# Kernel optimization log

Measured on AMD Instinct MI355X. Metric: run time of the kernel, lower is better.

## Reference

```python
import jax, jax.numpy as jnp
import numpy as np

B, L, H, D, TXT = 128, 512, 336, 256, 768
K, S, EMB = 16, 4, 128
H_SCALE = 0.15
EPS, ITERS = 0.05, 30
ALPHA, BETA = 1.0, 0.5
GW, TAU = 0.5, 0.07
LMB_MSE, LMB_COT, LMB_DELTA, LMB_ENT, LMB_TV = 1.0, 0.1, 0.1, 0.01, 0.01


def setup_inputs() -> dict:
    key = jax.random.key(0)
    ks = jax.random.split(key, 12)
    def xav(k, shape):
        return jax.random.normal(k, shape, jnp.float32) / np.sqrt(shape[0]).astype(np.float32)
    inp = {}
    inp['y_res'] = jax.random.normal(ks[0], (B, H, D), jnp.float32)
    inp['text_emb'] = jax.random.normal(ks[1], (B, TXT), jnp.float32)
    inp['enc_out'] = jax.random.normal(ks[2], (B, L, D), jnp.float32)
    inp['y_future'] = jax.random.normal(ks[3], (B, H, D), jnp.float32)
    inp['perm'] = jax.random.permutation(ks[4], EMB)
    inp['W_t2k'] = xav(ks[5], (TXT, K * (3 + S))); inp['b_t2k'] = jnp.zeros((K * (3 + S),), jnp.float32)
    inp['W_kemb'] = xav(ks[6], (H, EMB)); inp['b_kemb'] = jnp.zeros((EMB,), jnp.float32)
    inp['W_tir'] = xav(ks[7], (1, D)); inp['b_tir'] = jnp.zeros((D,), jnp.float32)
    inp['var_proj'] = jnp.ones((D,), jnp.float32)
    inp['W_g1'] = xav(ks[8], (2 * D + TXT, 512)); inp['b_g1'] = jnp.zeros((512,), jnp.float32)
    inp['W_g2'] = xav(ks[9], (512, D)); inp['b_g2'] = jnp.zeros((D,), jnp.float32)
    inp['W_fp'] = xav(ks[10], (3 * D, EMB)); inp['b_fp'] = jnp.zeros((EMB,), jnp.float32)
    return inp


def _text2kernels(text_emb, W, b):
    # text -> K temporal kernels: mixture of S shape bases with learned mu/sigma/amp
    raw = (text_emb @ W + b).reshape(-1, K, 3 + S)
    mu = jax.nn.sigmoid(raw[..., 0])                       # [B,K] center in [0,1]
    sig = jax.nn.softplus(raw[..., 1]) * H_SCALE + 1e-3     # [B,K] width
    amp = jax.nn.softplus(raw[..., 2])                      # [B,K]
    shape_w = jax.nn.softmax(raw[..., 3:], axis=-1)         # [B,K,S]
    t = (jnp.arange(H, dtype=text_emb.dtype) + 0.5) / H     # [H]
    z = (t[None, None, :] - mu[..., None]) / sig[..., None]  # [B,K,H]
    az = jnp.abs(z)
    in_supp = (az <= 1.0).astype(z.dtype)
    basis = jnp.stack([
        jnp.exp(-0.5 * z * z),
        jnp.exp(-az),
        jnp.maximum(1.0 - az, 0.0),
        0.5 * (1.0 + jnp.cos(jnp.pi * jnp.clip(z, -1.0, 1.0))) * in_supp,
    ], axis=-1)                                             # [B,K,H,S]
    kappa = amp[..., None] * jnp.einsum('bkhs,bks->bkh', basis, shape_w)
    return kappa, mu, shape_w


def _future_proj(y, W, b):
    # concat(y, first diff, second diff) -> linear, in_dim = 3*D
    d1 = jnp.diff(y, axis=1, prepend=y[:, :1])
    d2 = jnp.diff(d1, axis=1, prepend=d1[:, :1])
    return jnp.concatenate([y, d1, d2], axis=-1) @ W + b    # [B,H,EMB]


def _l2n(x):
    return x / (jnp.linalg.norm(x, axis=-1, keepdims=True) + 1e-8)


def _causal_cost(k_emb, f_pos, mu):
    cossim = jnp.einsum('bkd,bhd->bkh', _l2n(k_emb), _l2n(f_pos))
    t = (jnp.arange(H, dtype=k_emb.dtype) + 0.5) / H
    causal = jnp.maximum(mu[:, :, None] - t[None, None, :], 0.0)  # effect-before-cause penalty
    return ALPHA * (1.0 - cossim) + BETA * causal            # [B,K,H]


def _sinkhorn(C, r, c):
    Kmat = jnp.exp(-C / EPS)
    def body(i, uv):
        u, v = uv
        u = r / (jnp.einsum('bkh,bh->bk', Kmat, v) + 1e-9)
        v = c / (jnp.einsum('bkh,bk->bh', Kmat, u) + 1e-9)
        return (u, v)
    u, v = jax.lax.fori_loop(0, ITERS, body, (jnp.ones_like(r), jnp.ones_like(c)))
    return u[:, :, None] * Kmat * v[:, None, :]              # [B,K,H]


def _delta_contrastive(k_emb, f_pos, Pi, negatives):
    w = Pi / (jnp.sum(Pi, axis=-1, keepdims=True) + 1e-9)    # transport-weighted aggregation
    kn = _l2n(k_emb)
    def sim(f):
        return jnp.einsum('bkd,bkd->bk', kn, _l2n(jnp.einsum('bkh,bhd->bkd', w, f)))
    logits = jnp.stack([sim(f_pos)] + [sim(f) for f in negatives], axis=-1) / TAU  # [B,K,1+neg]
    return -jnp.mean(jax.nn.log_softmax(logits, axis=-1)[..., 0])


def reference(y_res, text_emb, enc_out, y_future, perm, W_t2k, b_t2k, W_kemb, b_kemb,
              W_tir, b_tir, var_proj, W_g1, b_g1, W_g2, b_g2, W_fp, b_fp):
    # --- text-induced response ---
    kappa, mu, shape_w = _text2kernels(text_emb, W_t2k, b_t2k)   # [B,K,H]
    y_tir_scalar = kappa.sum(axis=1)                             # [B,H]
    # --- gated fusion ---
    y_tir = (y_tir_scalar[..., None] @ W_tir + b_tir) * var_proj[None, None, :]  # [B,H,D]
    ts_global = enc_out.mean(axis=1)                             # [B,D]
    gate_in = jnp.concatenate([ts_global, text_emb, jnp.broadcast_to(var_proj[None, :], (y_res.shape[0], D))], axis=-1)
    gate = jax.nn.sigmoid(jax.nn.relu(gate_in @ W_g1 + b_g1) @ W_g2 + b_g2)[:, None, :]  # [B,1,D]
    y_hat = y_res + GW * gate * (y_tir - y_res)
    # --- aux losses ---
    k_emb = kappa @ W_kemb + b_kemb                              # [B,K,EMB]
    f_pos = _future_proj(y_future, W_fp, b_fp)                   # [B,H,EMB]
    C = _causal_cost(k_emb, f_pos, mu)
    r = jax.lax.stop_gradient(kappa.sum(-1) + 1e-6)
    r = r / r.sum(axis=-1, keepdims=True)
    c = jnp.full((C.shape[0], C.shape[2]), 1.0 / C.shape[2], C.dtype)
    Pi = _sinkhorn(C, r, c)
    shift = max(1, H // 6)
    f_neg1 = jnp.roll(f_pos, shift, axis=1)
    f_neg2 = f_pos[..., perm]
    loss_delta = _delta_contrastive(k_emb, f_pos, Pi, [f_neg1, f_neg2])
    loss_cot = jnp.mean(jnp.sum(C * Pi, axis=(1, 2)))
    sw = jnp.maximum(shape_w, 1e-8)
    loss_ent = -jnp.mean(jnp.sum(sw * jnp.log(sw), axis=-1))
    loss_tv = jnp.mean(jnp.abs(mu[:, 1:] - mu[:, :-1]))
    loss_mse = jnp.mean((y_hat - y_future) ** 2)
    return (LMB_MSE * loss_mse + LMB_COT * loss_cot + LMB_DELTA * loss_delta
            + LMB_ENT * loss_ent + LMB_TV * loss_tv)
```

## Files before the change

kernel.cpp:

```cpp
#include <hip/hip_runtime.h>
#include <math.h>

#define Bn   128
#define Ln   512
#define Hn   336
#define Dn   256
#define TXTn 768
#define Kn   16
#define EMBn 128
#define SHIFT 56
#define MSEB 1024
#define FROWS 48
#define FTILES 7
#define ASTRIDE 776

typedef __attribute__((ext_vector_type(8))) short short8;
typedef __attribute__((ext_vector_type(4))) float floatx4;

__device__ __forceinline__ float softplusf(float x){
  return fmaxf(x, 0.f) + log1pf(expf(-fabsf(x)));
}
__device__ __forceinline__ unsigned short f2bf(float x){
  unsigned int u = __float_as_uint(x);
  unsigned int r = (u + 0x7fffu + ((u >> 16) & 1u)) >> 16;
  return (unsigned short)r;
}
__device__ __forceinline__ float rcpf(float x){ return __builtin_amdgcn_rcpf(x); }
__device__ __forceinline__ float wsum(float x){
  x += __shfl_xor(x, 1);  x += __shfl_xor(x, 2);  x += __shfl_xor(x, 4);
  x += __shfl_xor(x, 8);  x += __shfl_xor(x, 16); x += __shfl_xor(x, 32);
  return x;
}

__global__ __launch_bounds__(256) void k_fused1(
    const float* __restrict__ text, const float* __restrict__ W, const float* __restrict__ bb,
    float* __restrict__ mu_o, float* __restrict__ kapT, float* __restrict__ rr_o,
    float* __restrict__ ytirs, float* __restrict__ part_ent, float* __restrict__ part_tv){
  int b = blockIdx.x, t = threadIdx.x;
  __shared__ float kapS[Kn*Hn];
  __shared__ float musL[Kn], sigL[Kn], ampL[Kn], shwL[Kn*4], entS[Kn], rrS[Kn];
  __shared__ float red[256];
  __shared__ float comb[112];
  __shared__ float totS;
  {
    int o = t & 127, half = t >> 7;
    if (o < 112){
      const float* tb = text + (size_t)b*TXTn + half*384;
      const float* Wb = W + (size_t)half*384*112 + o;
      float a0=0.f, a1=0.f, a2=0.f, a3=0.f;
      for (int i = 0; i < 384; i += 4){
        float4 x = *(const float4*)(tb + i);
        a0 += x.x*Wb[(i+0)*112]; a1 += x.y*Wb[(i+1)*112];
        a2 += x.z*Wb[(i+2)*112]; a3 += x.w*Wb[(i+3)*112];
      }
      red[half*112 + o] = (a0 + a1) + (a2 + a3);
    }
  }
  __syncthreads();
  if (t < 112) comb[t] = red[t] + red[112 + t] + bb[t];
  __syncthreads();
  if (t < Kn){
    float r0 = comb[t*7+0], r1 = comb[t*7+1], r2 = comb[t*7+2];
    float mu  = 1.f/(1.f+expf(-r0));
    float sig = softplusf(r1)*0.15f + 1e-3f;
    float amp = softplusf(r2);
    float s0 = comb[t*7+3], s1 = comb[t*7+4], s2 = comb[t*7+5], s3 = comb[t*7+6];
    float m = fmaxf(fmaxf(s0,s1), fmaxf(s2,s3));
    float e0 = expf(s0-m), e1 = expf(s1-m), e2 = expf(s2-m), e3 = expf(s3-m);
    float inv = 1.f/(e0+e1+e2+e3);
    float w0 = e0*inv, w1 = e1*inv, w2 = e2*inv, w3 = e3*inv;
    musL[t] = mu; sigL[t] = sig; ampL[t] = amp;
    shwL[t*4+0] = w0; shwL[t*4+1] = w1; shwL[t*4+2] = w2; shwL[t*4+3] = w3;
    mu_o[b*Kn + t] = mu;
    float ent = 0.f, sw;
    sw = fmaxf(w0,1e-8f); ent += sw*logf(sw);
    sw = fmaxf(w1,1e-8f); ent += sw*logf(sw);
    sw = fmaxf(w2,1e-8f); ent += sw*logf(sw);
    sw = fmaxf(w3,1e-8f); ent += sw*logf(sw);
    entS[t] = ent;
  }
  __syncthreads();
  for (int p = t; p < Kn*Hn; p += 256){
    int k = p/Hn, h = p - k*Hn;
    float mu = musL[k], sig = sigL[k], amp = ampL[k];
    float w0 = shwL[k*4+0], w1 = shwL[k*4+1], w2 = shwL[k*4+2], w3 = shwL[k*4+3];
    float tt = (h + 0.5f)/(float)Hn;
    float z  = (tt - mu)/sig;
    float az = fabsf(z);
    float b0 = expf(-0.5f*z*z);
    float b1 = expf(-az);
    float b2 = fmaxf(1.f-az, 0.f);
    float zc = fminf(fmaxf(z,-1.f),1.f);
    float b3 = (az <= 1.f) ? 0.5f*(1.f+cosf(3.14159265358979f*zc)) : 0.f;
    kapS[p] = amp*(w0*b0 + w1*b1 + w2*b2 + w3*b3);
  }
  __syncthreads();
  for (int q = t; q < Kn*Hn; q += 256){
    int h = q >> 4, k = q & 15;
    kapT[((size_t)b*Hn + h)*Kn + k] = kapS[k*Hn + h];
  }
  {
    int k = t >> 4, j16 = t & 15;
    float s = 0.f;
    for (int h = j16; h < Hn; h += 16) s += kapS[k*Hn + h];
    red[t] = s;
  }
  __syncthreads();
  if (t < Kn){
    float s = 0.f;
    for (int j = 0; j < 16; ++j) s += red[t*16 + j];
    rrS[t] = s + 1e-6f;
  }
  __syncthreads();
  if (t == 0){
    float tot = 0.f, tv = 0.f, es = 0.f;
    for (int k = 0; k < Kn; ++k) tot += rrS[k];
    for (int k = 1; k < Kn; ++k) tv += fabsf(musL[k]-musL[k-1]);
    for (int k = 0; k < Kn; ++k) es += entS[k];
    totS = tot; part_tv[b] = tv; part_ent[b] = es;
  }
  __syncthreads();
  if (t < Kn) rr_o[b*Kn + t] = rrS[t]/totS;
  for (int h = t; h < Hn; h += 256){
    float s = 0.f;
    #pragma unroll
    for (int k = 0; k < Kn; ++k) s += kapS[k*Hn + h];
    ytirs[b*Hn + h] = s;
  }
}

__global__ __launch_bounds__(128) void k_kemb1(const float* __restrict__ kapT,
    const float* __restrict__ W, float* __restrict__ kp){
  int blk = blockIdx.x;
  int b = blk >> 3, oc = blk & 7;
  int e = threadIdx.x;
  float acc[Kn];
  #pragma unroll
  for (int k = 0; k < Kn; ++k) acc[k] = 0.f;
  const float* kb = kapT + (size_t)b*Hn*Kn;
  int h0 = oc*42, h1 = h0 + 42;
  for (int h = h0; h < h1; ++h){
    float wv = W[h*EMBn + e];
    const float4* kr = (const float4*)(kb + h*Kn);
    float4 c0 = kr[0], c1 = kr[1], c2 = kr[2], c3 = kr[3];
    acc[0]  += c0.x*wv; acc[1]  += c0.y*wv; acc[2]  += c0.z*wv; acc[3]  += c0.w*wv;
    acc[4]  += c1.x*wv; acc[5]  += c1.y*wv; acc[6]  += c1.z*wv; acc[7]  += c1.w*wv;
    acc[8]  += c2.x*wv; acc[9]  += c2.y*wv; acc[10] += c2.z*wv; acc[11] += c2.w*wv;
    acc[12] += c3.x*wv; acc[13] += c3.y*wv; acc[14] += c3.z*wv; acc[15] += c3.w*wv;
  }
  float* kpb = kp + ((size_t)blk*Kn)*EMBn + e;
  #pragma unroll
  for (int k = 0; k < Kn; ++k) kpb[(size_t)k*EMBn] = acc[k];
}

__global__ __launch_bounds__(256) void k_kemb2(const float* __restrict__ kp,
    const float* __restrict__ bb, float* __restrict__ kn_o){
  int b = blockIdx.x, t = threadIdx.x;
  __shared__ float kS[Kn*EMBn];
  __shared__ float r2[256];
  __shared__ float invS[Kn];
  for (int j = t; j < Kn*EMBn; j += 256){
    int e = j & 127;
    float s = bb[e];
    const float* p = kp + (size_t)b*8*Kn*EMBn + j;
    #pragma unroll
    for (int oc = 0; oc < 8; ++oc) s += p[(size_t)oc*Kn*EMBn];
    kS[j] = s;
  }
  __syncthreads();
  {
    int k = t & 15, g = t >> 4;
    float s = 0.f;
    for (int e = g; e < EMBn; e += 16){ float v = kS[k*EMBn + e]; s += v*v; }
    r2[g*Kn + k] = s;
  }
  __syncthreads();
  if (t < Kn){
    float s = 0.f;
    for (int g = 0; g < 16; ++g) s += r2[g*Kn + t];
    invS[t] = 1.f/(sqrtf(s) + 1e-8f);
  }
  __syncthreads();
  for (int j = t; j < Kn*EMBn; j += 256)
    kn_o[(size_t)b*Kn*EMBn + j] = kS[j]*invS[j >> 7];
}

__global__ void k_wprep(const float* __restrict__ W, unsigned short* __restrict__ Bsw){
  int tid = blockIdx.x*256 + threadIdx.x;
  int k = tid >> 7, n = tid & 127;
  int kt = k >> 5, kr = k & 31, quad = kr >> 3, j = kr & 7;
  int c = n >> 4, ln = n & 15;
  int lane = quad*16 + ln;
  int dst = ((kt*8 + c)*64 + lane)*8 + j;
  Bsw[dst] = f2bf(W[k*128 + n]);
}

__global__ __launch_bounds__(256) void k_encmean(const float* __restrict__ enc,
                                                 float* __restrict__ psum){
  int blk = blockIdx.x;
  int b = blk >> 3, p = blk & 7;
  int t = threadIdx.x;
  int d4 = t & 63, rg = t >> 6;
  const float4* e4 = (const float4*)(enc + (size_t)b*Ln*Dn);
  float4 s = make_float4(0.f,0.f,0.f,0.f);
  for (int l = p + 8*rg; l < Ln; l += 32){
    float4 v = e4[(size_t)l*64 + d4];
    s.x += v.x; s.y += v.y; s.z += v.z; s.w += v.w;
  }
  __shared__ float4 red[256];
  red[t] = s;
  __syncthreads();
  if (rg == 0){
    float4 o = red[d4];
    #pragma unroll
    for (int r = 1; r < 4; ++r){
      float4 v = red[r*64 + d4];
      o.x += v.x; o.y += v.y; o.z += v.z; o.w += v.w;
    }
    ((float4*)(psum + ((size_t)b*8 + p)*Dn))[d4] = o;
  }
}

__global__ __launch_bounds__(256) void k_gmlp1(const float* __restrict__ psum,
    const float* __restrict__ text, const float* __restrict__ vp,
    const float* __restrict__ W1, float* __restrict__ hidp){
  int bt = blockIdx.x >> 5, hc = (blockIdx.x >> 2) & 7, ks = blockIdx.x & 3;
  int t = threadIdx.x;
  __shared__ float inS[4][320];
  for (int j = t; j < 4*320; j += 256){
    int bi = j / 320, jj = j - bi*320;
    int gi = ks*320 + jj;
    int b = bt*4 + bi;
    float vsl;
    if (gi < Dn){
      float s = 0.f;
      for (int p = 0; p < 8; ++p) s += psum[((size_t)b*8 + p)*Dn + gi];
      vsl = s * (1.f/(float)Ln);
    } else if (gi < Dn + TXTn){
      vsl = text[(size_t)b*TXTn + (gi - Dn)];
    } else {
      vsl = vp[gi - Dn - TXTn];
    }
    inS[bi][jj] = vsl;
  }
  __syncthreads();
  int h = t & 63, bi = t >> 6;
  int hidx = hc*64 + h;
  const float* Wb = W1 + (size_t)(ks*320)*512 + hidx;
  float a0 = 0.f, a1 = 0.f, a2 = 0.f, a3 = 0.f;
  const float4* in4 = (const float4*)inS[bi];
  for (int i = 0; i < 320; i += 4){
    float4 x = in4[i >> 2];
    a0 += x.x*Wb[(size_t)(i+0)*512]; a1 += x.y*Wb[(size_t)(i+1)*512];
    a2 += x.z*Wb[(size_t)(i+2)*512]; a3 += x.w*Wb[(size_t)(i+3)*512];
  }
  hidp[((size_t)ks*Bn + bt*4 + bi)*512 + hidx] = (a0 + a1) + (a2 + a3);
}

__global__ __launch_bounds__(256) void k_gmlp2(const float* __restrict__ hidp,
    const float* __restrict__ b1, const float* __restrict__ W2,
    const float* __restrict__ b2, float* __restrict__ gate_o){
  int bt = blockIdx.x >> 3, dc = blockIdx.x & 7;
  int t = threadIdx.x;
  __shared__ float hS[4][512];
  __shared__ float pS[8][4][32];
  for (int j = t; j < 4*512; j += 256){
    int bi = j >> 9, i = j & 511;
    size_t bidx = (size_t)(bt*4 + bi)*512 + i;
    float s = hidp[bidx] + hidp[(size_t)Bn*512 + bidx]
            + hidp[(size_t)2*Bn*512 + bidx] + hidp[(size_t)3*Bn*512 + bidx];
    hS[bi][i] = fmaxf(s + b1[i], 0.f);
  }
  __syncthreads();
  {
    int dl = t & 31, ig = t >> 5;
    int d  = dc*32 + dl;
    float a0=0.f, a1=0.f, a2=0.f, a3=0.f;
    int i0 = ig*64;
    for (int i = i0; i < i0 + 64; ++i){
      float wv = W2[(size_t)i*Dn + d];
      a0 += hS[0][i]*wv; a1 += hS[1][i]*wv;
      a2 += hS[2][i]*wv; a3 += hS[3][i]*wv;
    }
    pS[ig][0][dl] = a0; pS[ig][1][dl] = a1;
    pS[ig][2][dl] = a2; pS[ig][3][dl] = a3;
  }
  __syncthreads();
  if (t < 128){
    int bi = t >> 5, dl = t & 31;
    float s = 0.f;
    #pragma unroll
    for (int g = 0; g < 8; ++g) s += pS[g][bi][dl];
    s += b2[dc*32 + dl];
    gate_o[(size_t)(bt*4 + bi)*Dn + dc*32 + dl] = 1.f/(1.f + expf(-s));
  }
}

__global__ __launch_bounds__(256) void k_fposm(const float* __restrict__ yf,
    const unsigned short* __restrict__ Bsw, const float* __restrict__ bb,
    float* __restrict__ fpos, float* __restrict__ finv){
  int b = blockIdx.x / FTILES, tile = blockIdx.x % FTILES;
  int t = threadIdx.x;
  int h0 = tile*FROWS;
  __shared__ unsigned short yS[FROWS*ASTRIDE];
  __shared__ float rsq[4][FROWS];
  const float* yb = yf + (size_t)b*Hn*Dn;

  #pragma unroll
  for (int u = 0; u < 12; ++u){
    int unit = t + 256*u;
    int r = unit >> 6, d4 = unit & 63;
    int h = h0 + r;
    int hm1 = h-1 < 0 ? 0 : h-1;
    int hm2 = h-2 < 0 ? 0 : h-2;
    float4 y   = *(const float4*)(yb + (size_t)h  *Dn + d4*4);
    float4 ym1 = *(const float4*)(yb + (size_t)hm1*Dn + d4*4);
    float4 ym2 = *(const float4*)(yb + (size_t)hm2*Dn + d4*4);
    float4 d1 = make_float4(y.x-ym1.x, y.y-ym1.y, y.z-ym1.z, y.w-ym1.w);
    float4 d2 = make_float4(y.x-2.f*ym1.x+ym2.x, y.y-2.f*ym1.y+ym2.y,
                            y.z-2.f*ym1.z+ym2.z, y.w-2.f*ym1.w+ym2.w);
    union { unsigned short u16[4]; uint2 v; } p;
    unsigned short* base = &yS[r*ASTRIDE + d4*4];
    p.u16[0]=f2bf(y.x);  p.u16[1]=f2bf(y.y);  p.u16[2]=f2bf(y.z);  p.u16[3]=f2bf(y.w);
    *(uint2*)(base)        = p.v;
    p.u16[0]=f2bf(d1.x); p.u16[1]=f2bf(d1.y); p.u16[2]=f2bf(d1.z); p.u16[3]=f2bf(d1.w);
    *(uint2*)(base + 256)  = p.v;
    p.u16[0]=f2bf(d2.x); p.u16[1]=f2bf(d2.y); p.u16[2]=f2bf(d2.z); p.u16[3]=f2bf(d2.w);
    *(uint2*)(base + 512)  = p.v;
  }
  __syncthreads();

  int wv   = __builtin_amdgcn_readfirstlane(t >> 6);
  int lane = t & 63, quad = lane >> 4, ln = lane & 15;
  int c0 = wv*2;
  floatx4 acc[3][2];
  #pragma unroll
  for (int i = 0; i < 3; ++i){
    acc[i][0] = (floatx4){0.f,0.f,0.f,0.f};
    acc[i][1] = (floatx4){0.f,0.f,0.f,0.f};
  }
  #pragma unroll
  for (int kt = 0; kt < 24; ++kt){
    int aoff = kt*32 + quad*8;
    short8 a0 = *(const short8*)&yS[( 0 + ln)*ASTRIDE + aoff];
    short8 a1 = *(const short8*)&yS[(16 + ln)*ASTRIDE + aoff];
    short8 a2 = *(const short8*)&yS[(32 + ln)*ASTRIDE + aoff];
    short8 b0 = *(const short8*)&Bsw[((kt*8 + c0  )*64 + lane)*8];
    short8 b1 = *(const short8*)&Bsw[((kt*8 + c0+1)*64 + lane)*8];
    acc[0][0] = __builtin_amdgcn_mfma_f32_16x16x32_bf16(a0, b0, acc[0][0], 0, 0, 0);
    acc[0][1] = __builtin_amdgcn_mfma_f32_16x16x32_bf16(a0, b1, acc[0][1], 0, 0, 0);
    acc[1][0] = __builtin_amdgcn_mfma_f32_16x16x32_bf16(a1, b0, acc[1][0], 0, 0, 0);
    acc[1][1] = __builtin_amdgcn_mfma_f32_16x16x32_bf16(a1, b1, acc[1][1], 0, 0, 0);
    acc[2][0] = __builtin_amdgcn_mfma_f32_16x16x32_bf16(a2, b0, acc[2][0], 0, 0, 0);
    acc[2][1] = __builtin_amdgcn_mfma_f32_16x16x32_bf16(a2, b1, acc[2][1], 0, 0, 0);
  }

  float bias0 = bb[c0*16 + ln], bias1 = bb[(c0+1)*16 + ln];
  #pragma unroll
  for (int rt = 0; rt < 3; ++rt){
    #pragma unroll
    for (int reg = 0; reg < 4; ++reg){
      int lrow = rt*16 + quad*4 + reg;
      size_t row = (size_t)b*Hn + h0 + lrow;
      float v0 = acc[rt][0][reg] + bias0;
      float v1 = acc[rt][1][reg] + bias1;
      fpos[row*EMBn + c0*16 + ln]     = v0;
      fpos[row*EMBn + (c0+1)*16 + ln] = v1;
      float sq = v0*v0 + v1*v1;
      sq += __shfl_xor(sq, 1); sq += __shfl_xor(sq, 2);
      sq += __shfl_xor(sq, 4); sq += __shfl_xor(sq, 8);
      if (ln == 0) rsq[wv][lrow] = sq;
    }
  }
  __syncthreads();
  if (t < FROWS){
    float s = rsq[0][t] + rsq[1][t] + rsq[2][t] + rsq[3][t];
    finv[(size_t)b*Hn + h0 + t] = 1.f/(sqrtf(s) + 1e-8f);
  }
}

__global__ void k_mse(const float* __restrict__ yres, const float* __restrict__ yfut,
                      const float* __restrict__ gate, const float* __restrict__ ytirs,
                      const float* __restrict__ Wt, const float* __restrict__ bt,
                      const float* __restrict__ vp, float* __restrict__ part_mse){
  const long long total = (long long)Bn*Hn*Dn;
  long long tid = blockIdx.x*(long long)blockDim.x + threadIdx.x;
  long long nth = gridDim.x*(long long)blockDim.x;
  float part = 0.f;
  for (long long i4 = tid; i4*4 < total; i4 += nth){
    long long base = i4*4;
    int b = (int)(base/((long long)Hn*Dn));
    int rem = (int)(base - (long long)b*Hn*Dn);
    int h = rem/Dn, d = rem - h*Dn;
    float4 yr = *(const float4*)(yres + base);
    float4 yv = *(const float4*)(yfut + base);
    float4 g  = *(const float4*)(gate + (size_t)b*Dn + d);
    float4 wt = *(const float4*)(Wt + d);
    float4 bv = *(const float4*)(bt + d);
    float4 vv = *(const float4*)(vp + d);
    float ys = ytirs[b*Hn + h];
    float yt, yh, e;
    yt = (ys*wt.x + bv.x)*vv.x; yh = yr.x + 0.5f*g.x*(yt-yr.x); e = yh-yv.x; part += e*e;
    yt = (ys*wt.y + bv.y)*vv.y; yh = yr.y + 0.5f*g.y*(yt-yr.y); e = yh-yv.y; part += e*e;
    yt = (ys*wt.z + bv.z)*vv.z; yh = yr.z + 0.5f*g.z*(yt-yr.z); e = yh-yv.z; part += e*e;
    yt = (ys*wt.w + bv.w)*vv.w; yh = yr.w + 0.5f*g.w*(yt-yr.w); e = yh-yv.w; part += e*e;
  }
  __shared__ float red[256];
  red[threadIdx.x] = part; __syncthreads();
  for (int s = 128; s > 0; s >>= 1){
    if (threadIdx.x < s) red[threadIdx.x] += red[threadIdx.x + s];
    __syncthreads();
  }
  if (threadIdx.x == 0) part_mse[blockIdx.x] = red[0];
}

__global__ __launch_bounds__(256) void k_cost(const float* __restrict__ kn,
    const float* __restrict__ fpos, const float* __restrict__ finv,
    const float* __restrict__ mu_i, float* __restrict__ Km_g){
  int b = blockIdx.x >> 2, q = blockIdx.x & 3;
  int t = threadIdx.x;
  __shared__ float knS[Kn*132];
  __shared__ float musS[Kn];
  for (int j = t; j < Kn*EMBn; j += 256){
    int k = j >> 7, e = j & 127;
    knS[k*132 + e] = kn[(size_t)b*Kn*EMBn + j];
  }
  if (t < Kn) musS[t] = mu_i[b*Kn + t];
  __syncthreads();
  const int H0 = q*84;
  for (int p = t; p < Kn*84; p += 256){
    int k = p & 15, h = H0 + (p >> 4);
    const float4* f4 = (const float4*)(fpos + ((size_t)b*Hn + h)*EMBn);
    const float4* k4 = (const float4*)(knS + k*132);
    float s = 0.f;
    #pragma unroll 8
    for (int i = 0; i < EMBn/4; ++i){
      float4 a = k4[i], f = f4[i];
      s += a.x*f.x + a.y*f.y + a.z*f.z + a.w*f.w;
    }
    float cs = s*finv[b*Hn + h];
    float th = (h + 0.5f)/(float)Hn;
    float c  = (1.f - cs) + 0.5f*fmaxf(musS[k] - th, 0.f);
    Km_g[(size_t)b*Kn*Hn + k*Hn + h] = expf(-20.f*c);
  }
}

__global__ __launch_bounds__(128) void k_sink1w(const float* __restrict__ rr,
    float* KmwT, float* __restrict__ part_cot){
  int b = blockIdx.x, t = threadIdx.x;
  int l = t & 63;
  float* Kb = KmwT + (size_t)b*Kn*Hn;
  int ks = ((l&1)<<3) | ((l&2)<<1) | ((l&4)>>1) | ((l&8)>>3);
  __shared__ float ws[128];
  float km[16][3];
  #pragma unroll
  for (int m = 0; m < 16; ++m){
    const float* rowp = Kb + (size_t)(ks ^ m)*Hn;
    #pragma unroll
    for (int c = 0; c < 3; ++c){
      int h = 128*c + t;
      km[m][c] = (h < Hn) ? rowp[h] : 0.f;
    }
  }
  float rrl = rr[b*Kn + ks];
  float v[3];
  v[0] = 1.f; v[1] = 1.f; v[2] = 1.f;
  float w[16];
  for (int it = 0; it < 30; ++it){
    float p[16];
    #pragma unroll
    for (int m = 0; m < 16; ++m)
      p[m] = km[m][0]*v[0] + km[m][1]*v[1] + km[m][2]*v[2];
    #pragma unroll
    for (int m = 0; m < 8; ++m) p[m] += __shfl_xor(p[m+8], 1);
    #pragma unroll
    for (int m = 0; m < 4; ++m) p[m] += __shfl_xor(p[m+4], 2);
    #pragma unroll
    for (int m = 0; m < 2; ++m) p[m] += __shfl_xor(p[m+2], 4);
    p[0] += __shfl_xor(p[1], 8);
    p[0] += __shfl_xor(p[0], 16);
    p[0] += __shfl_xor(p[0], 32);
    ws[t] = p[0];
    __syncthreads();
    float ptot = ws[l] + ws[64 + l];
    __syncthreads();
    float ul = rrl * rcpf(ptot + 1e-9f);
    w[0] = ul;
    w[1] = __shfl_xor(w[0], 8);
    w[2] = __shfl_xor(w[0], 4); w[3] = __shfl_xor(w[1], 4);
    #pragma unroll
    for (int j = 0; j < 4; ++j) w[4+j] = __shfl_xor(w[j], 2);
    #pragma unroll
    for (int j = 0; j < 8; ++j) w[8+j] = __shfl_xor(w[j], 1);
    #pragma unroll
    for (int c = 0; c < 3; ++c){
      float s0 = 0.f, s1 = 0.f;
      #pragma unroll
      for (int m = 0; m < 8; ++m){ s0 += km[m][c]*w[m]; s1 += km[m+8][c]*w[m+8]; }
      v[c] = (1.f/(float)Hn) * rcpf(s0 + s1 + 1e-9f);
    }
  }
  float q[16];
  #pragma unroll
  for (int m = 0; m < 16; ++m)
    q[m] = km[m][0]*v[0] + km[m][1]*v[1] + km[m][2]*v[2];
  #pragma unroll
  for (int m = 0; m < 8; ++m) q[m] += __shfl_xor(q[m+8], 1);
  #pragma unroll
  for (int m = 0; m < 4; ++m) q[m] += __shfl_xor(q[m+4], 2);
  #pragma unroll
  for (int m = 0; m < 2; ++m) q[m] += __shfl_xor(q[m+2], 4);
  q[0] += __shfl_xor(q[1], 8);
  q[0] += __shfl_xor(q[0], 16);
  q[0] += __shfl_xor(q[0], 32);
  ws[t] = q[0];
  __syncthreads();
  float qtot = ws[l] + ws[64 + l];
  __syncthreads();
  float tt[16];
  tt[0] = qtot;
  tt[1] = __shfl_xor(tt[0], 8);
  tt[2] = __shfl_xor(tt[0], 4); tt[3] = __shfl_xor(tt[1], 4);
  #pragma unroll
  for (int j = 0; j < 4; ++j) tt[4+j] = __shfl_xor(tt[j], 2);
  #pragma unroll
  for (int j = 0; j < 8; ++j) tt[8+j] = __shfl_xor(tt[j], 1);
  float cot = 0.f;
  #pragma unroll
  for (int m = 0; m < 16; ++m){
    float rsinv = rcpf(w[m]*tt[m] + 1e-9f);
    float* rowp = Kb + (size_t)(ks ^ m)*Hn;
    #pragma unroll
    for (int c = 0; c < 3; ++c){
      int h = 128*c + t;
      if (h < Hn){
        float Pi = w[m]*km[m][c]*v[c];
        cot += (-0.05f)*logf(km[m][c])*Pi;
        rowp[h] = Pi*rsinv;
      }
    }
  }
  cot = wsum(cot);
  ws[t] = cot;
  __syncthreads();
  if (t == 0) part_cot[b] = ws[0] + ws[64];
}

__global__ __launch_bounds__(256) void k_agg(const float* __restrict__ kn,
    const float* __restrict__ fpos, const float* __restrict__ wT,
    const int* __restrict__ perm, float* __restrict__ part_del4){
  int b = blockIdx.x >> 2, kg = blockIdx.x & 3;
  int t = threadIdx.x;
  __shared__ float wTl[Hn*4];
  __shared__ float apH[2][4*EMBn];
  __shared__ float a1H[2][4*EMBn];
  __shared__ int permS[EMBn];
  __shared__ float redW[4];
  if (t < EMBn) permS[t] = perm[t];
  for (int j = t; j < 4*Hn; j += 256){
    int k = j & 3, h = j >> 2;
    wTl[h*4 + k] = wT[(size_t)b*Kn*Hn + (size_t)(kg*4 + k)*Hn + h];
  }
  __syncthreads();

  {
    int e = t & 127, jh = t >> 7;
    float ap[4], a1[4];
    #pragma unroll
    for (int j = 0; j < 4; ++j){ ap[j] = 0.f; a1[j] = 0.f; }
    const float* fb = fpos + (size_t)b*Hn*EMBn + e;
    int hh0 = jh*168, hh1 = hh0 + 168;
    for (int h = hh0; h < hh1; ++h){
      float fv = fb[(size_t)h*EMBn];
      int h1 = h + SHIFT; if (h1 >= Hn) h1 -= Hn;
      float4 wA = *(const float4*)&wTl[h *4];
      float4 wB = *(const float4*)&wTl[h1*4];
      ap[0] += wA.x*fv; ap[1] += wA.y*fv; ap[2] += wA.z*fv; ap[3] += wA.w*fv;
      a1[0] += wB.x*fv; a1[1] += wB.y*fv; a1[2] += wB.z*fv; a1[3] += wB.w*fv;
    }
    #pragma unroll
    for (int j = 0; j < 4; ++j){
      apH[jh][j*EMBn + e] = ap[j];
      a1H[jh][j*EMBn + e] = a1[j];
    }
  }
  __syncthreads();
  for (int j = t; j < 4*EMBn; j += 256){
    apH[0][j] += apH[1][j];
    a1H[0][j] += a1H[1][j];
  }
  __syncthreads();

  int wave = t >> 6, lane = t & 63;
  {
    int kl = wave;
    int k  = kg*4 + kl;
    float sp = 0.f, s1 = 0.f, s2 = 0.f, np = 0.f, n1 = 0.f;
    for (int e = lane; e < EMBn; e += 64){
      float kne = kn[((size_t)b*Kn + k)*EMBn + e];
      float a  = apH[0][kl*EMBn + e];
      float c1 = a1H[0][kl*EMBn + e];
      sp += kne*a; s1 += kne*c1;
      s2 += kne*apH[0][kl*EMBn + permS[e]];
      np += a*a; n1 += c1*c1;
    }
    for (int o = 32; o; o >>= 1){
      sp += __shfl_down(sp, o); s1 += __shfl_down(s1, o); s2 += __shfl_down(s2, o);
      np += __shfl_down(np, o); n1 += __shfl_down(n1, o);
    }
    if (lane == 0){
      float ip  = 1.f/(sqrtf(np) + 1e-8f);
      float i1v = 1.f/(sqrtf(n1) + 1e-8f);
      const float ti = 1.f/0.07f;
      float l0 = sp*ip*ti, l1 = s1*i1v*ti, l2 = s2*ip*ti;
      float m = fmaxf(l0, fmaxf(l1, l2));
      float lse = m + logf(expf(l0-m) + expf(l1-m) + expf(l2-m));
      redW[wave] = lse - l0;
    }
  }
  __syncthreads();
  if (t == 0) part_del4[(size_t)b*4 + kg] = redW[0] + redW[1] + redW[2] + redW[3];
}

__global__ void k_final(const float* __restrict__ part_mse, const float* __restrict__ part_cot,
                        const float* __restrict__ part_del4, const float* __restrict__ part_ent,
                        const float* __restrict__ part_tv, float* __restrict__ out){
  int t = threadIdx.x;
  __shared__ double sred[256];
  double m = 0.0;
  for (int i = t; i < MSEB; i += 256) m += (double)part_mse[i];
  double o4 = 0.0;
  if (t < Bn){
    double del = (double)part_del4[4*t] + (double)part_del4[4*t + 1]
               + (double)part_del4[4*t + 2] + (double)part_del4[4*t + 3];
    o4 = 0.1*(double)part_cot[t] + (0.1/(double)Kn)*del
       - (0.01/(double)Kn)*(double)part_ent[t] + (0.01/(double)(Kn-1))*(double)part_tv[t];
  }
  sred[t] = m/((double)Bn*Hn*Dn) + o4/(double)Bn;
  __syncthreads();
  for (int s = 128; s > 0; s >>= 1){ if (t < s) sred[t] += sred[t+s]; __syncthreads(); }
  if (t == 0) out[0] = (float)sred[0];
}

extern "C" void kernel_launch(void* const* d_in, const int* in_sizes, int n_in,
                              void* d_out, int out_size, void* d_ws, size_t ws_size,
                              hipStream_t stream) {
  const float* y_res  = (const float*)d_in[0];
  const float* text   = (const float*)d_in[1];
  const float* enc    = (const float*)d_in[2];
  const float* yfut   = (const float*)d_in[3];
  const int*   perm   = (const int*)  d_in[4];
  const float* W_t2k  = (const float*)d_in[5];
  const float* b_t2k  = (const float*)d_in[6];
  const float* W_kemb = (const float*)d_in[7];
  const float* b_kemb = (const float*)d_in[8];
  const float* W_tir  = (const float*)d_in[9];
  const float* b_tir  = (const float*)d_in[10];
  const float* vproj  = (const float*)d_in[11];
  const float* W_g1   = (const float*)d_in[12];
  const float* b_g1   = (const float*)d_in[13];
  const float* W_g2   = (const float*)d_in[14];
  const float* b_g2   = (const float*)d_in[15];
  const float* W_fp   = (const float*)d_in[16];
  const float* b_fp   = (const float*)d_in[17];

  float* F = (float*)d_ws;
  float* mu_w   = F;
  float* rr_w   = F + 2048;
  float* ytr_w  = F + 4096;
  float* kapT_w = F + 47104;
  float* kn_w   = F + 735232;
  float* gate_w = F + 997376;
  float* fp_w   = F + 1030144;
  float* fi_w   = F + 6535168;
  float* pmse_w = F + 6578176;
  float* pcot_w = F + 6579200;
  float* pent_w = F + 6579456;
  float* ptv_w  = F + 6579584;
  unsigned short* Bsw_w = (unsigned short*)kapT_w;
  float* KmwT_w = kapT_w;
  float* kp_w   = fp_w;
  float* psum_w = fp_w;
  float* hidp_w = fp_w + 262144;
  float* pdel4_w = gate_w;

  k_fused1 <<<Bn, 256, 0, stream>>>(text, W_t2k, b_t2k, mu_w, kapT_w, rr_w, ytr_w, pent_w, ptv_w);
  k_kemb1  <<<Bn*8, 128, 0, stream>>>(kapT_w, W_kemb, kp_w);
  k_kemb2  <<<Bn, 256, 0, stream>>>(kp_w, b_kemb, kn_w);
  k_wprep  <<<384, 256, 0, stream>>>(W_fp, Bsw_w);
  k_encmean<<<Bn*8, 256, 0, stream>>>(enc, psum_w);
  k_gmlp1  <<<1024, 256, 0, stream>>>(psum_w, text, vproj, W_g1, hidp_w);
  k_gmlp2  <<<256, 256, 0, stream>>>(hidp_w, b_g1, W_g2, b_g2, gate_w);
  k_fposm  <<<Bn*FTILES, 256, 0, stream>>>(yfut, Bsw_w, b_fp, fp_w, fi_w);
  k_mse    <<<MSEB, 256, 0, stream>>>(y_res, yfut, gate_w, ytr_w, W_tir, b_tir, vproj, pmse_w);
  k_cost   <<<Bn*4, 256, 0, stream>>>(kn_w, fp_w, fi_w, mu_w, KmwT_w);
  k_sink1w <<<Bn, 128, 0, stream>>>(rr_w, KmwT_w, pcot_w);
  k_agg    <<<Bn*4, 256, 0, stream>>>(kn_w, fp_w, KmwT_w, perm, pdel4_w);
  k_final  <<<1, 256, 0, stream>>>(pmse_w, pcot_w, pdel4_w, pent_w, ptv_w, (float*)d_out);
}
```

Before: 346.0 us.

## Merge independent kernels into multi-role launches to cut launch count

Independent kernels are grouped into combined launches that branch on block index: kemb normalization, weight swizzle and encoder mean share one launch; gate MLP layer 1 and the future projection MFMA share another; gate layer 2 and the cost computation share a third; MSE and the contrastive aggregation share a fourth. This cuts the launch count from 13 to 8 and lets unrelated work overlap on the GPU. Scratch buffers for psum, hidp and pdel4 move to dedicated workspace regions so the merged stages no longer alias each other. The merged launches size shared memory for the largest role, which may lower occupancy for the smaller roles.

```diff
diff --git a/kernel.cpp b/kernel.cpp
--- a/kernel.cpp
+++ b/kernel.cpp
@@ -153,295 +153,260 @@
   for (int k = 0; k < Kn; ++k) kpb[(size_t)k*EMBn] = acc[k];
 }
 
-__global__ __launch_bounds__(256) void k_kemb2(const float* __restrict__ kp,
-    const float* __restrict__ bb, float* __restrict__ kn_o){
-  int b = blockIdx.x, t = threadIdx.x;
+__global__ __launch_bounds__(256) void k_p3(const float* __restrict__ kp,
+    const float* __restrict__ bkemb, float* __restrict__ kn_o,
+    const float* __restrict__ Wfp, unsigned short* __restrict__ Bsw,
+    const float* __restrict__ enc, float* __restrict__ psum){
+  int blk = blockIdx.x, t = threadIdx.x;
   __shared__ float kS[Kn*EMBn];
   __shared__ float r2[256];
   __shared__ float invS[Kn];
-  for (int j = t; j < Kn*EMBn; j += 256){
-    int e = j & 127;
-    float s = bb[e];
-    const float* p = kp + (size_t)b*8*Kn*EMBn + j;
-    #pragma unroll
-    for (int oc = 0; oc < 8; ++oc) s += p[(size_t)oc*Kn*EMBn];
-    kS[j] = s;
-  }
-  __syncthreads();
-  {
-    int k = t & 15, g = t >> 4;
-    float s = 0.f;
-    for (int e = g; e < EMBn; e += 16){ float v = kS[k*EMBn + e]; s += v*v; }
-    r2[g*Kn + k] = s;
-  }
-  __syncthreads();
-  if (t < Kn){
-    float s = 0.f;
-    for (int g = 0; g < 16; ++g) s += r2[g*Kn + t];
-    invS[t] = 1.f/(sqrtf(s) + 1e-8f);
-  }
-  __syncthreads();
-  for (int j = t; j < Kn*EMBn; j += 256)
-    kn_o[(size_t)b*Kn*EMBn + j] = kS[j]*invS[j >> 7];
-}
-
-__global__ void k_wprep(const float* __restrict__ W, unsigned short* __restrict__ Bsw){
-  int tid = blockIdx.x*256 + threadIdx.x;
-  int k = tid >> 7, n = tid & 127;
-  int kt = k >> 5, kr = k & 31, quad = kr >> 3, j = kr & 7;
-  int c = n >> 4, ln = n & 15;
-  int lane = quad*16 + ln;
-  int dst = ((kt*8 + c)*64 + lane)*8 + j;
-  Bsw[dst] = f2bf(W[k*128 + n]);
-}
-
-__global__ __launch_bounds__(256) void k_encmean(const float* __restrict__ enc,
-                                                 float* __restrict__ psum){
-  int blk = blockIdx.x;
-  int b = blk >> 3, p = blk & 7;
-  int t = threadIdx.x;
-  int d4 = t & 63, rg = t >> 6;
-  const float4* e4 = (const float4*)(enc + (size_t)b*Ln*Dn);
-  float4 s = make_float4(0.f,0.f,0.f,0.f);
-  for (int l = p + 8*rg; l < Ln; l += 32){
-    float4 v = e4[(size_t)l*64 + d4];
-    s.x += v.x; s.y += v.y; s.z += v.z; s.w += v.w;
-  }
-  __shared__ float4 red[256];
-  red[t] = s;
-  __syncthreads();
-  if (rg == 0){
-    float4 o = red[d4];
-    #pragma unroll
-    for (int r = 1; r < 4; ++r){
-      float4 v = red[r*64 + d4];
-      o.x += v.x; o.y += v.y; o.z += v.z; o.w += v.w;
-    }
-    ((float4*)(psum + ((size_t)b*8 + p)*Dn))[d4] = o;
-  }
-}
-
-__global__ __launch_bounds__(256) void k_gmlp1(const float* __restrict__ psum,
+  __shared__ float4 redE[256];
+  if (blk < 128){
+    int b = blk;
+    for (int j = t; j < Kn*EMBn; j += 256){
+      int e = j & 127;
+      float s = bkemb[e];
+      const float* p = kp + (size_t)b*8*Kn*EMBn + j;
+      #pragma unroll
+      for (int oc = 0; oc < 8; ++oc) s += p[(size_t)oc*Kn*EMBn];
+      kS[j] = s;
+    }
+    __syncthreads();
+    {
+      int k = t & 15, g = t >> 4;
+      float s = 0.f;
+      for (int e = g; e < EMBn; e += 16){ float v = kS[k*EMBn + e]; s += v*v; }
+      r2[g*Kn + k] = s;
+    }
+    __syncthreads();
+    if (t < Kn){
+      float s = 0.f;
+      for (int g = 0; g < 16; ++g) s += r2[g*Kn + t];
+      invS[t] = 1.f/(sqrtf(s) + 1e-8f);
+    }
+    __syncthreads();
+    for (int j = t; j < Kn*EMBn; j += 256)
+      kn_o[(size_t)blk*Kn*EMBn + j] = kS[j]*invS[j >> 7];
+  } else if (blk < 512){
+    int tid = (blk - 128)*256 + t;
+    int k = tid >> 7, n = tid & 127;
+    int kt = k >> 5, kr = k & 31, quad = kr >> 3, j = kr & 7;
+    int c = n >> 4, ln = n & 15;
+    int lane = quad*16 + ln;
+    int dst = ((kt*8 + c)*64 + lane)*8 + j;
+    Bsw[dst] = f2bf(Wfp[k*128 + n]);
+  } else {
+    int eb = blk - 512;
+    int b = eb >> 3, p = eb & 7;
+    int d4 = t & 63, rg = t >> 6;
+    const float4* e4 = (const float4*)(enc + (size_t)b*Ln*Dn);
+    float4 s = make_float4(0.f,0.f,0.f,0.f);
+    for (int l = p + 8*rg; l < Ln; l += 32){
+      float4 v = e4[(size_t)l*64 + d4];
+      s.x += v.x; s.y += v.y; s.z += v.z; s.w += v.w;
+    }
+    redE[t] = s;
+    __syncthreads();
+    if (rg == 0){
+      float4 o = redE[d4];
+      #pragma unroll
+      for (int r = 1; r < 4; ++r){
+        float4 v = redE[r*64 + d4];
+        o.x += v.x; o.y += v.y; o.z += v.z; o.w += v.w;
+      }
+      ((float4*)(psum + ((size_t)b*8 + p)*Dn))[d4] = o;
+    }
+  }
+}
+
+__global__ __launch_bounds__(256) void k_p4(const float* __restrict__ psum,
     const float* __restrict__ text, const float* __restrict__ vp,
-    const float* __restrict__ W1, float* __restrict__ hidp){
-  int bt = blockIdx.x >> 5, hc = (blockIdx.x >> 2) & 7, ks = blockIdx.x & 3;
-  int t = threadIdx.x;
-  __shared__ float inS[4][320];
-  for (int j = t; j < 4*320; j += 256){
-    int bi = j / 320, jj = j - bi*320;
-    int gi = ks*320 + jj;
-    int b = bt*4 + bi;
-    float vsl;
-    if (gi < Dn){
-      float s = 0.f;
-      for (int p = 0; p < 8; ++p) s += psum[((size_t)b*8 + p)*Dn + gi];
-      vsl = s * (1.f/(float)Ln);
-    } else if (gi < Dn + TXTn){
-      vsl = text[(size_t)b*TXTn + (gi - Dn)];
-    } else {
-      vsl = vp[gi - Dn - TXTn];
-    }
-    inS[bi][jj] = vsl;
-  }
-  __syncthreads();
-  int h = t & 63, bi = t >> 6;
-  int hidx = hc*64 + h;
-  const float* Wb = W1 + (size_t)(ks*320)*512 + hidx;
-  float a0 = 0.f, a1 = 0.f, a2 = 0.f, a3 = 0.f;
-  const float4* in4 = (const float4*)inS[bi];
-  for (int i = 0; i < 320; i += 4){
-    float4 x = in4[i >> 2];
-    a0 += x.x*Wb[(size_t)(i+0)*512]; a1 += x.y*Wb[(size_t)(i+1)*512];
-    a2 += x.z*Wb[(size_t)(i+2)*512]; a3 += x.w*Wb[(size_t)(i+3)*512];
-  }
-  hidp[((size_t)ks*Bn + bt*4 + bi)*512 + hidx] = (a0 + a1) + (a2 + a3);
-}
-
-__global__ __launch_bounds__(256) void k_gmlp2(const float* __restrict__ hidp,
+    const float* __restrict__ W1, float* __restrict__ hidp,
+    const float* __restrict__ yf, const unsigned short* __restrict__ Bsw,
+    const float* __restrict__ bfp, float* __restrict__ fpos, float* __restrict__ finv){
+  int blk = blockIdx.x, t = threadIdx.x;
+  __shared__ __align__(16) unsigned char smem[FROWS*ASTRIDE*2 + 4*FROWS*4];
+  if (blk < 1024){
+    float (*inS)[320] = (float(*)[320])smem;
+    int bt = blk >> 5, hc = (blk >> 2) & 7, ks = blk & 3;
+    for (int j = t; j < 4*320; j += 256){
+      int bi = j / 320, jj = j - bi*320;
+      int gi = ks*320 + jj;
+      int b = bt*4 + bi;
+      float vsl;
+      if (gi < Dn){
+        float s = 0.f;
+        for (int p = 0; p < 8; ++p) s += psum[((size_t)b*8 + p)*Dn + gi];
+        vsl = s * (1.f/(float)Ln);
+      } else if (gi < Dn + TXTn){
+        vsl = text[(size_t)b*TXTn + (gi - Dn)];
+      } else {
+        vsl = vp[gi - Dn - TXTn];
+      }
+      inS[bi][jj] = vsl;
+    }
+    __syncthreads();
+    int h = t & 63, bi = t >> 6;
+    int hidx = hc*64 + h;
+    const float* Wb = W1 + (size_t)(ks*320)*512 + hidx;
+    float a0 = 0.f, a1 = 0.f, a2 = 0.f, a3 = 0.f;
+    const float4* in4 = (const float4*)inS[bi];
+    for (int i = 0; i < 320; i += 4){
+      float4 x = in4[i >> 2];
+      a0 += x.x*Wb[(size_t)(i+0)*512]; a1 += x.y*Wb[(size_t)(i+1)*512];
+      a2 += x.z*Wb[(size_t)(i+2)*512]; a3 += x.w*Wb[(size_t)(i+3)*512];
+    }
+    hidp[((size_t)ks*Bn + bt*4 + bi)*512 + hidx] = (a0 + a1) + (a2 + a3);
+  } else {
+    unsigned short* yS = (unsigned short*)smem;
+    float (*rsq)[FROWS] = (float(*)[FROWS])(smem + FROWS*ASTRIDE*2);
+    int idx = blk - 1024;
+    int b = idx / FTILES, tile = idx % FTILES;
+    int h0 = tile*FROWS;
+    const float* yb = yf + (size_t)b*Hn*Dn;
+    #pragma unroll
+    for (int u = 0; u < 12; ++u){
+      int unit = t + 256*u;
+      int r = unit >> 6, d4 = unit & 63;
+      int h = h0 + r;
+      int hm1 = h-1 < 0 ? 0 : h-1;
+      int hm2 = h-2 < 0 ? 0 : h-2;
+      float4 y   = *(const float4*)(yb + (size_t)h  *Dn + d4*4);
+      float4 ym1 = *(const float4*)(yb + (size_t)hm1*Dn + d4*4);
+      float4 ym2 = *(const float4*)(yb + (size_t)hm2*Dn + d4*4);
+      float4 d1 = make_float4(y.x-ym1.x, y.y-ym1.y, y.z-ym1.z, y.w-ym1.w);
+      float4 d2 = make_float4(y.x-2.f*ym1.x+ym2.x, y.y-2.f*ym1.y+ym2.y,
+                              y.z-2.f*ym1.z+ym2.z, y.w-2.f*ym1.w+ym2.w);
+      union { unsigned short u16[4]; uint2 v; } p;
+      unsigned short* base = &yS[r*ASTRIDE + d4*4];
+      p.u16[0]=f2bf(y.x);  p.u16[1]=f2bf(y.y);  p.u16[2]=f2bf(y.z);  p.u16[3]=f2bf(y.w);
+      *(uint2*)(base)        = p.v;
+      p.u16[0]=f2bf(d1.x); p.u16[1]=f2bf(d1.y); p.u16[2]=f2bf(d1.z); p.u16[3]=f2bf(d1.w);
+      *(uint2*)(base + 256)  = p.v;
+      p.u16[0]=f2bf(d2.x); p.u16[1]=f2bf(d2.y); p.u16[2]=f2bf(d2.z); p.u16[3]=f2bf(d2.w);
+      *(uint2*)(base + 512)  = p.v;
+    }
+    __syncthreads();
+
+    int wv   = __builtin_amdgcn_readfirstlane(t >> 6);
+    int lane = t & 63, quad = lane >> 4, ln = lane & 15;
+    int c0 = wv*2;
+    floatx4 acc[3][2];
+    #pragma unroll
+    for (int i = 0; i < 3; ++i){
+      acc[i][0] = (floatx4){0.f,0.f,0.f,0.f};
+      acc[i][1] = (floatx4){0.f,0.f,0.f,0.f};
+    }
+    #pragma unroll
+    for (int kt = 0; kt < 24; ++kt){
+      int aoff = kt*32 + quad*8;
+      short8 a0 = *(const short8*)&yS[( 0 + ln)*ASTRIDE + aoff];
+      short8 a1 = *(const short8*)&yS[(16 + ln)*ASTRIDE + aoff];
+      short8 a2 = *(const short8*)&yS[(32 + ln)*ASTRIDE + aoff];
+      short8 b0 = *(const short8*)&Bsw[((kt*8 + c0  )*64 + lane)*8];
+      short8 b1 = *(const short8*)&Bsw[((kt*8 + c0+1)*64 + lane)*8];
+      acc[0][0] = __builtin_amdgcn_mfma_f32_16x16x32_bf16(a0, b0, acc[0][0], 0, 0, 0);
+      acc[0][1] = __builtin_amdgcn_mfma_f32_16x16x32_bf16(a0, b1, acc[0][1], 0, 0, 0);
+      acc[1][0] = __builtin_amdgcn_mfma_f32_16x16x32_bf16(a1, b0, acc[1][0], 0, 0, 0);
+      acc[1][1] = __builtin_amdgcn_mfma_f32_16x16x32_bf16(a1, b1, acc[1][1], 0, 0, 0);
+      acc[2][0] = __builtin_amdgcn_mfma_f32_16x16x32_bf16(a2, b0, acc[2][0], 0, 0, 0);
+      acc[2][1] = __builtin_amdgcn_mfma_f32_16x16x32_bf16(a2, b1, acc[2][1], 0, 0, 0);
+    }
+
+    float bias0 = bfp[c0*16 + ln], bias1 = bfp[(c0+1)*16 + ln];
+    #pragma unroll
+    for (int rt = 0; rt < 3; ++rt){
+      #pragma unroll
+      for (int reg = 0; reg < 4; ++reg){
+        int lrow = rt*16 + quad*4 + reg;
+        size_t row = (size_t)b*Hn + h0 + lrow;
+        float v0 = acc[rt][0][reg] + bias0;
+        float v1 = acc[rt][1][reg] + bias1;
+        fpos[row*EMBn + c0*16 + ln]     = v0;
+        fpos[row*EMBn + (c0+1)*16 + ln] = v1;
+        float sq = v0*v0 + v1*v1;
+        sq += __shfl_xor(sq, 1); sq += __shfl_xor(sq, 2);
+        sq += __shfl_xor(sq, 4); sq += __shfl_xor(sq, 8);
+        if (ln == 0) rsq[wv][lrow] = sq;
+      }
+    }
+    __syncthreads();
+    if (t < FROWS){
+      float s = rsq[0][t] + rsq[1][t] + rsq[2][t] + rsq[3][t];
+      finv[(size_t)b*Hn + h0 + t] = 1.f/(sqrtf(s) + 1e-8f);
+    }
+  }
+}
+
+__global__ __launch_bounds__(256) void k_p5(const float* __restrict__ hidp,
     const float* __restrict__ b1, const float* __restrict__ W2,
-    const float* __restrict__ b2, float* __restrict__ gate_o){
-  int bt = blockIdx.x >> 3, dc = blockIdx.x & 7;
-  int t = threadIdx.x;
+    const float* __restrict__ b2, float* __restrict__ gate_o,
+    const float* __restrict__ kn, const float* __restrict__ fpos,
+    const float* __restrict__ finv, const float* __restrict__ mu_i,
+    float* __restrict__ Km_g){
+  int blk = blockIdx.x, t = threadIdx.x;
   __shared__ float hS[4][512];
   __shared__ float pS[8][4][32];
-  for (int j = t; j < 4*512; j += 256){
-    int bi = j >> 9, i = j & 511;
-    size_t bidx = (size_t)(bt*4 + bi)*512 + i;
-    float s = hidp[bidx] + hidp[(size_t)Bn*512 + bidx]
-            + hidp[(size_t)2*Bn*512 + bidx] + hidp[(size_t)3*Bn*512 + bidx];
-    hS[bi][i] = fmaxf(s + b1[i], 0.f);
-  }
-  __syncthreads();
-  {
-    int dl = t & 31, ig = t >> 5;
-    int d  = dc*32 + dl;
-    float a0=0.f, a1=0.f, a2=0.f, a3=0.f;
-    int i0 = ig*64;
-    for (int i = i0; i < i0 + 64; ++i){
-      float wv = W2[(size_t)i*Dn + d];
-      a0 += hS[0][i]*wv; a1 += hS[1][i]*wv;
-      a2 += hS[2][i]*wv; a3 += hS[3][i]*wv;
-    }
-    pS[ig][0][dl] = a0; pS[ig][1][dl] = a1;
-    pS[ig][2][dl] = a2; pS[ig][3][dl] = a3;
-  }
-  __syncthreads();
-  if (t < 128){
-    int bi = t >> 5, dl = t & 31;
-    float s = 0.f;
-    #pragma unroll
-    for (int g = 0; g < 8; ++g) s += pS[g][bi][dl];
-    s += b2[dc*32 + dl];
-    gate_o[(size_t)(bt*4 + bi)*Dn + dc*32 + dl] = 1.f/(1.f + expf(-s));
-  }
-}
-
-__global__ __launch_bounds__(256) void k_fposm(const float* __restrict__ yf,
-    const unsigned short* __restrict__ Bsw, const float* __restrict__ bb,
-    float* __restrict__ fpos, float* __restrict__ finv){
-  int b = blockIdx.x / FTILES, tile = blockIdx.x % FTILES;
-  int t = threadIdx.x;
-  int h0 = tile*FROWS;
-  __shared__ unsigned short yS[FROWS*ASTRIDE];
-  __shared__ float rsq[4][FROWS];
-  const float* yb = yf + (size_t)b*Hn*Dn;
-
-  #pragma unroll
-  for (int u = 0; u < 12; ++u){
-    int unit = t + 256*u;
-    int r = unit >> 6, d4 = unit & 63;
-    int h = h0 + r;
-    int hm1 = h-1 < 0 ? 0 : h-1;
-    int hm2 = h-2 < 0 ? 0 : h-2;
-    float4 y   = *(const float4*)(yb + (size_t)h  *Dn + d4*4);
-    float4 ym1 = *(const float4*)(yb + (size_t)hm1*Dn + d4*4);
-    float4 ym2 = *(const float4*)(yb + (size_t)hm2*Dn + d4*4);
-    float4 d1 = make_float4(y.x-ym1.x, y.y-ym1.y, y.z-ym1.z, y.w-ym1.w);
-    float4 d2 = make_float4(y.x-2.f*ym1.x+ym2.x, y.y-2.f*ym1.y+ym2.y,
-                            y.z-2.f*ym1.z+ym2.z, y.w-2.f*ym1.w+ym2.w);
-    union { unsigned short u16[4]; uint2 v; } p;
-    unsigned short* base = &yS[r*ASTRIDE + d4*4];
-    p.u16[0]=f2bf(y.x);  p.u16[1]=f2bf(y.y);  p.u16[2]=f2bf(y.z);  p.u16[3]=f2bf(y.w);
-    *(uint2*)(base)        = p.v;
-    p.u16[0]=f2bf(d1.x); p.u16[1]=f2bf(d1.y); p.u16[2]=f2bf(d1.z); p.u16[3]=f2bf(d1.w);
-    *(uint2*)(base + 256)  = p.v;
-    p.u16[0]=f2bf(d2.x); p.u16[1]=f2bf(d2.y); p.u16[2]=f2bf(d2.z); p.u16[3]=f2bf(d2.w);
-    *(uint2*)(base + 512)  = p.v;
-  }
-  __syncthreads();
-
-  int wv   = __builtin_amdgcn_readfirstlane(t >> 6);
-  int lane = t & 63, quad = lane >> 4, ln = lane & 15;
-  int c0 = wv*2;
-  floatx4 acc[3][2];
-  #pragma unroll
-  for (int i = 0; i < 3; ++i){
-    acc[i][0] = (floatx4){0.f,0.f,0.f,0.f};
-    acc[i][1] = (floatx4){0.f,0.f,0.f,0.f};
-  }
-  #pragma unroll
-  for (int kt = 0; kt < 24; ++kt){
-    int aoff = kt*32 + quad*8;
-    short8 a0 = *(const short8*)&yS[( 0 + ln)*ASTRIDE + aoff];
-    short8 a1 = *(const short8*)&yS[(16 + ln)*ASTRIDE + aoff];
-    short8 a2 = *(const short8*)&yS[(32 + ln)*ASTRIDE + aoff];
-    short8 b0 = *(const short8*)&Bsw[((kt*8 + c0  )*64 + lane)*8];
-    short8 b1 = *(const short8*)&Bsw[((kt*8 + c0+1)*64 + lane)*8];
-    acc[0][0] = __builtin_amdgcn_mfma_f32_16x16x32_bf16(a0, b0, acc[0][0], 0, 0, 0);
-    acc[0][1] = __builtin_amdgcn_mfma_f32_16x16x32_bf16(a0, b1, acc[0][1], 0, 0, 0);
-    acc[1][0] = __builtin_amdgcn_mfma_f32_16x16x32_bf16(a1, b0, acc[1][0], 0, 0, 0);
-    acc[1][1] = __builtin_amdgcn_mfma_f32_16x16x32_bf16(a1, b1, acc[1][1], 0, 0, 0);
-    acc[2][0] = __builtin_amdgcn_mfma_f32_16x16x32_bf16(a2, b0, acc[2][0], 0, 0, 0);
-    acc[2][1] = __builtin_amdgcn_mfma_f32_16x16x32_bf16(a2, b1, acc[2][1], 0, 0, 0);
-  }
-
-  float bias0 = bb[c0*16 + ln], bias1 = bb[(c0+1)*16 + ln];
-  #pragma unroll
-  for (int rt = 0; rt < 3; ++rt){
-    #pragma unroll
-    for (int reg = 0; reg < 4; ++reg){
-      int lrow = rt*16 + quad*4 + reg;
-      size_t row = (size_t)b*Hn + h0 + lrow;
-      float v0 = acc[rt][0][reg] + bias0;
-      float v1 = acc[rt][1][reg] + bias1;
-      fpos[row*EMBn + c0*16 + ln]     = v0;
-      fpos[row*EMBn + (c0+1)*16 + ln] = v1;
-      float sq = v0*v0 + v1*v1;
-      sq += __shfl_xor(sq, 1); sq += __shfl_xor(sq, 2);
-      sq += __shfl_xor(sq, 4); sq += __shfl_xor(sq, 8);
-      if (ln == 0) rsq[wv][lrow] = sq;
-    }
-  }
-  __syncthreads();
-  if (t < FROWS){
-    float s = rsq[0][t] + rsq[1][t] + rsq[2][t] + rsq[3][t];
-    finv[(size_t)b*Hn + h0 + t] = 1.f/(sqrtf(s) + 1e-8f);
-  }
-}
-
-__global__ void k_mse(const float* __restrict__ yres, const float* __restrict__ yfut,
-                      const float* __restrict__ gate, const float* __restrict__ ytirs,
-                      const float* __restrict__ Wt, const float* __restrict__ bt,
-                      const float* __restrict__ vp, float* __restrict__ part_mse){
-  const long long total = (long long)Bn*Hn*Dn;
-  long long tid = blockIdx.x*(long long)blockDim.x + threadIdx.x;
-  long long nth = gridDim.x*(long long)blockDim.x;
-  float part = 0.f;
-  for (long long i4 = tid; i4*4 < total; i4 += nth){
-    long long base = i4*4;
-    int b = (int)(base/((long long)Hn*Dn));
-    int rem = (int)(base - (long long)b*Hn*Dn);
-    int h = rem/Dn, d = rem - h*Dn;
-    float4 yr = *(const float4*)(yres + base);
-    float4 yv = *(const float4*)(yfut + base);
-    float4 g  = *(const float4*)(gate + (size_t)b*Dn + d);
-    float4 wt = *(const float4*)(Wt + d);
-    float4 bv = *(const float4*)(bt + d);
-    float4 vv = *(const float4*)(vp + d);
-    float ys = ytirs[b*Hn + h];
-    float yt, yh, e;
-    yt = (ys*wt.x + bv.x)*vv.x; yh = yr.x + 0.5f*g.x*(yt-yr.x); e = yh-yv.x; part += e*e;
-    yt = (ys*wt.y + bv.y)*vv.y; yh = yr.y + 0.5f*g.y*(yt-yr.y); e = yh-yv.y; part += e*e;
-    yt = (ys*wt.z + bv.z)*vv.z; yh = yr.z + 0.5f*g.z*(yt-yr.z); e = yh-yv.z; part += e*e;
-    yt = (ys*wt.w + bv.w)*vv.w; yh = yr.w + 0.5f*g.w*(yt-yr.w); e = yh-yv.w; part += e*e;
-  }
-  __shared__ float red[256];
-  red[threadIdx.x] = part; __syncthreads();
-  for (int s = 128; s > 0; s >>= 1){
-    if (threadIdx.x < s) red[threadIdx.x] += red[threadIdx.x + s];
-    __syncthreads();
-  }
-  if (threadIdx.x == 0) part_mse[blockIdx.x] = red[0];
-}
-
-__global__ __launch_bounds__(256) void k_cost(const float* __restrict__ kn,
-    const float* __restrict__ fpos, const float* __restrict__ finv,
-    const float* __restrict__ mu_i, float* __restrict__ Km_g){
-  int b = blockIdx.x >> 2, q = blockIdx.x & 3;
-  int t = threadIdx.x;
-  __shared__ float knS[Kn*132];
-  __shared__ float musS[Kn];
-  for (int j = t; j < Kn*EMBn; j += 256){
-    int k = j >> 7, e = j & 127;
-    knS[k*132 + e] = kn[(size_t)b*Kn*EMBn + j];
-  }
-  if (t < Kn) musS[t] = mu_i[b*Kn + t];
-  __syncthreads();
-  const int H0 = q*84;
-  for (int p = t; p < Kn*84; p += 256){
-    int k = p & 15, h = H0 + (p >> 4);
-    const float4* f4 = (const float4*)(fpos + ((size_t)b*Hn + h)*EMBn);
-    const float4* k4 = (const float4*)(knS + k*132);
-    float s = 0.f;
-    #pragma unroll 8
-    for (int i = 0; i < EMBn/4; ++i){
-      float4 a = k4[i], f = f4[i];
-      s += a.x*f.x + a.y*f.y + a.z*f.z + a.w*f.w;
-    }
-    float cs = s*finv[b*Hn + h];
-    float th = (h + 0.5f)/(float)Hn;
-    float c  = (1.f - cs) + 0.5f*fmaxf(musS[k] - th, 0.f);
-    Km_g[(size_t)b*Kn*Hn + k*Hn + h] = expf(-20.f*c);
+  if (blk < 256){
+    int bt = blk >> 3, dc = blk & 7;
+    for (int j = t; j < 4*512; j += 256){
+      int bi = j >> 9, i = j & 511;
+      size_t bidx = (size_t)(bt*4 + bi)*512 + i;
+      float s = hidp[bidx] + hidp[(size_t)Bn*512 + bidx]
+              + hidp[(size_t)2*Bn*512 + bidx] + hidp[(size_t)3*Bn*512 + bidx];
+      hS[bi][i] = fmaxf(s + b1[i], 0.f);
+    }
+    __syncthreads();
+    {
+      int dl = t & 31, ig = t >> 5;
+      int d  = dc*32 + dl;
+      float a0=0.f, a1=0.f, a2=0.f, a3=0.f;
+      int i0 = ig*64;
+      for (int i = i0; i < i0 + 64; ++i){
+        float wv = W2[(size_t)i*Dn + d];
+        a0 += hS[0][i]*wv; a1 += hS[1][i]*wv;
+        a2 += hS[2][i]*wv; a3 += hS[3][i]*wv;
+      }
+      pS[ig][0][dl] = a0; pS[ig][1][dl] = a1;
+      pS[ig][2][dl] = a2; pS[ig][3][dl] = a3;
+    }
+    __syncthreads();
+    if (t < 128){
+      int bi = t >> 5, dl = t & 31;
+      float s = 0.f;
+      #pragma unroll
+      for (int g = 0; g < 8; ++g) s += pS[g][bi][dl];
+      s += b2[dc*32 + dl];
+      gate_o[(size_t)(bt*4 + bi)*Dn + dc*32 + dl] = 1.f/(1.f + expf(-s));
+    }
+  } else {
+    float* knS = (float*)hS;
+    float* musS = ((float*)pS) + 0;
+    int cb = blk - 256;
+    int b = cb >> 2, q = cb & 3;
+    for (int j = t; j < Kn*EMBn; j += 256){
+      int k = j >> 7, e = j & 127;
+      knS[k*132 + e] = kn[(size_t)b*Kn*EMBn + j];
+    }
+    if (t < Kn) musS[t] = mu_i[b*Kn + t];
+    __syncthreads();
+    const int H0 = q*84;
+    for (int p = t; p < Kn*84; p += 256){
+      int k = p & 15, h = H0 + (p >> 4);
+      const float4* f4 = (const float4*)(fpos + ((size_t)b*Hn + h)*EMBn);
+      const float4* k4 = (const float4*)(knS + k*132);
+      float s = 0.f;
+      #pragma unroll 8
+      for (int i = 0; i < EMBn/4; ++i){
+        float4 a = k4[i], f = f4[i];
+        s += a.x*f.x + a.y*f.y + a.z*f.z + a.w*f.w;
+      }
+      float cs = s*finv[b*Hn + h];
+      float th = (h + 0.5f)/(float)Hn;
+      float c  = (1.f - cs) + 0.5f*fmaxf(musS[k] - th, 0.f);
+      Km_g[(size_t)b*Kn*Hn + k*Hn + h] = expf(-20.f*c);
+    }
   }
 }
 
@@ -546,80 +511,116 @@
   if (t == 0) part_cot[b] = ws[0] + ws[64];
 }
 
-__global__ __launch_bounds__(256) void k_agg(const float* __restrict__ kn,
-    const float* __restrict__ fpos, const float* __restrict__ wT,
-    const int* __restrict__ perm, float* __restrict__ part_del4){
-  int b = blockIdx.x >> 2, kg = blockIdx.x & 3;
-  int t = threadIdx.x;
+__global__ __launch_bounds__(256) void k_p7(const float* __restrict__ yres,
+    const float* __restrict__ yfut, const float* __restrict__ gate,
+    const float* __restrict__ ytirs, const float* __restrict__ Wt,
+    const float* __restrict__ bt, const float* __restrict__ vp,
+    float* __restrict__ part_mse,
+    const float* __restrict__ kn, const float* __restrict__ fpos,
+    const float* __restrict__ wT, const int* __restrict__ perm,
+    float* __restrict__ part_del4){
+  int blk = blockIdx.x, t = threadIdx.x;
+  __shared__ float redM[256];
   __shared__ float wTl[Hn*4];
   __shared__ float apH[2][4*EMBn];
   __shared__ float a1H[2][4*EMBn];
   __shared__ int permS[EMBn];
   __shared__ float redW[4];
-  if (t < EMBn) permS[t] = perm[t];
-  for (int j = t; j < 4*Hn; j += 256){
-    int k = j & 3, h = j >> 2;
-    wTl[h*4 + k] = wT[(size_t)b*Kn*Hn + (size_t)(kg*4 + k)*Hn + h];
-  }
-  __syncthreads();
-
-  {
-    int e = t & 127, jh = t >> 7;
-    float ap[4], a1[4];
-    #pragma unroll
-    for (int j = 0; j < 4; ++j){ ap[j] = 0.f; a1[j] = 0.f; }
-    const float* fb = fpos + (size_t)b*Hn*EMBn + e;
-    int hh0 = jh*168, hh1 = hh0 + 168;
-    for (int h = hh0; h < hh1; ++h){
-      float fv = fb[(size_t)h*EMBn];
-      int h1 = h + SHIFT; if (h1 >= Hn) h1 -= Hn;
-      float4 wA = *(const float4*)&wTl[h *4];
-      float4 wB = *(const float4*)&wTl[h1*4];
-      ap[0] += wA.x*fv; ap[1] += wA.y*fv; ap[2] += wA.z*fv; ap[3] += wA.w*fv;
-      a1[0] += wB.x*fv; a1[1] += wB.y*fv; a1[2] += wB.z*fv; a1[3] += wB.w*fv;
-    }
-    #pragma unroll
-    for (int j = 0; j < 4; ++j){
-      apH[jh][j*EMBn + e] = ap[j];
-      a1H[jh][j*EMBn + e] = a1[j];
-    }
-  }
-  __syncthreads();
-  for (int j = t; j < 4*EMBn; j += 256){
-    apH[0][j] += apH[1][j];
-    a1H[0][j] += a1H[1][j];
-  }
-  __syncthreads();
-
-  int wave = t >> 6, lane = t & 63;
-  {
-    int kl = wave;
-    int k  = kg*4 + kl;
-    float sp = 0.f, s1 = 0.f, s2 = 0.f, np = 0.f, n1 = 0.f;
-    for (int e = lane; e < EMBn; e += 64){
-      float kne = kn[((size_t)b*Kn + k)*EMBn + e];
-      float a  = apH[0][kl*EMBn + e];
-      float c1 = a1H[0][kl*EMBn + e];
-      sp += kne*a; s1 += kne*c1;
-      s2 += kne*apH[0][kl*EMBn + permS[e]];
-      np += a*a; n1 += c1*c1;
-    }
-    for (int o = 32; o; o >>= 1){
-      sp += __shfl_down(sp, o); s1 += __shfl_down(s1, o); s2 += __shfl_down(s2, o);
-      np += __shfl_down(np, o); n1 += __shfl_down(n1, o);
-    }
-    if (lane == 0){
-      float ip  = 1.f/(sqrtf(np) + 1e-8f);
-      float i1v = 1.f/(sqrtf(n1) + 1e-8f);
-      const float ti = 1.f/0.07f;
-      float l0 = sp*ip*ti, l1 = s1*i1v*ti, l2 = s2*ip*ti;
-      float m = fmaxf(l0, fmaxf(l1, l2));
-      float lse = m + logf(expf(l0-m) + expf(l1-m) + expf(l2-m));
-      redW[wave] = lse - l0;
-    }
-  }
-  __syncthreads();
-  if (t == 0) part_del4[(size_t)b*4 + kg] = redW[0] + redW[1] + redW[2] + redW[3];
+  if (blk < MSEB){
+    const long long total = (long long)Bn*Hn*Dn;
+    long long tid = blk*256LL + t;
+    const long long nth = (long long)MSEB*256;
+    float part = 0.f;
+    for (long long i4 = tid; i4*4 < total; i4 += nth){
+      long long base = i4*4;
+      int b = (int)(base/((long long)Hn*Dn));
+      int rem = (int)(base - (long long)b*Hn*Dn);
+      int h = rem/Dn, d = rem - h*Dn;
+      float4 yr = *(const float4*)(yres + base);
+      float4 yv = *(const float4*)(yfut + base);
+      float4 g  = *(const float4*)(gate + (size_t)b*Dn + d);
+      float4 wt = *(const float4*)(Wt + d);
+      float4 bv = *(const float4*)(bt + d);
+      float4 vv = *(const float4*)(vp + d);
+      float ys = ytirs[b*Hn + h];
+      float yt, yh, e;
+      yt = (ys*wt.x + bv.x)*vv.x; yh = yr.x + 0.5f*g.x*(yt-yr.x); e = yh-yv.x; part += e*e;
+      yt = (ys*wt.y + bv.y)*vv.y; yh = yr.y + 0.5f*g.y*(yt-yr.y); e = yh-yv.y; part += e*e;
+      yt = (ys*wt.z + bv.z)*vv.z; yh = yr.z + 0.5f*g.z*(yt-yr.z); e = yh-yv.z; part += e*e;
+      yt = (ys*wt.w + bv.w)*vv.w; yh = yr.w + 0.5f*g.w*(yt-yr.w); e = yh-yv.w; part += e*e;
+    }
+    redM[t] = part; __syncthreads();
+    for (int s = 128; s > 0; s >>= 1){
+      if (t < s) redM[t] += redM[t + s];
+      __syncthreads();
+    }
+    if (t == 0) part_mse[blk] = redM[0];
+  } else {
+    int ab = blk - MSEB;
+    int b = ab >> 2, kg = ab & 3;
+    if (t < EMBn) permS[t] = perm[t];
+    for (int j = t; j < 4*Hn; j += 256){
+      int k = j & 3, h = j >> 2;
+      wTl[h*4 + k] = wT[(size_t)b*Kn*Hn + (size_t)(kg*4 + k)*Hn + h];
+    }
+    __syncthreads();
+    {
+      int e = t & 127, jh = t >> 7;
+      float ap[4], a1[4];
+      #pragma unroll
+      for (int j = 0; j < 4; ++j){ ap[j] = 0.f; a1[j] = 0.f; }
+      const float* fb = fpos + (size_t)b*Hn*EMBn + e;
+      int hh0 = jh*168, hh1 = hh0 + 168;
+      for (int h = hh0; h < hh1; ++h){
+        float fv = fb[(size_t)h*EMBn];
+        int h1 = h + SHIFT; if (h1 >= Hn) h1 -= Hn;
+        float4 wA = *(const float4*)&wTl[h *4];
+        float4 wB = *(const float4*)&wTl[h1*4];
+        ap[0] += wA.x*fv; ap[1] += wA.y*fv; ap[2] += wA.z*fv; ap[3] += wA.w*fv;
+        a1[0] += wB.x*fv; a1[1] += wB.y*fv; a1[2] += wB.z*fv; a1[3] += wB.w*fv;
+      }
+      #pragma unroll
+      for (int j = 0; j < 4; ++j){
+        apH[jh][j*EMBn + e] = ap[j];
+        a1H[jh][j*EMBn + e] = a1[j];
+      }
+    }
+    __syncthreads();
+    for (int j = t; j < 4*EMBn; j += 256){
+      apH[0][j] += apH[1][j];
+      a1H[0][j] += a1H[1][j];
+    }
+    __syncthreads();
+    int wave = t >> 6, lane = t & 63;
+    {
+      int kl = wave;
+      int k  = kg*4 + kl;
+      float sp = 0.f, s1 = 0.f, s2 = 0.f, np = 0.f, n1 = 0.f;
+      for (int e = lane; e < EMBn; e += 64){
+        float kne = kn[((size_t)b*Kn + k)*EMBn + e];
+        float a  = apH[0][kl*EMBn + e];
+        float c1 = a1H[0][kl*EMBn + e];
+        sp += kne*a; s1 += kne*c1;
+        s2 += kne*apH[0][kl*EMBn + permS[e]];
+        np += a*a; n1 += c1*c1;
+      }
+      for (int o = 32; o; o >>= 1){
+        sp += __shfl_down(sp, o); s1 += __shfl_down(s1, o); s2 += __shfl_down(s2, o);
+        np += __shfl_down(np, o); n1 += __shfl_down(n1, o);
+      }
+      if (lane == 0){
+        float ip  = 1.f/(sqrtf(np) + 1e-8f);
+        float i1v = 1.f/(sqrtf(n1) + 1e-8f);
+        const float ti = 1.f/0.07f;
+        float l0 = sp*ip*ti, l1 = s1*i1v*ti, l2 = s2*ip*ti;
+        float m = fmaxf(l0, fmaxf(l1, l2));
+        float lse = m + logf(expf(l0-m) + expf(l1-m) + expf(l2-m));
+        redW[wave] = lse - l0;
+      }
+    }
+    __syncthreads();
+    if (t == 0) part_del4[(size_t)b*4 + kg] = redW[0] + redW[1] + redW[2] + redW[3];
+  }
 }
 
 __global__ void k_final(const float* __restrict__ part_mse, const float* __restrict__ part_cot,
@@ -677,24 +678,22 @@
   float* pcot_w = F + 6579200;
   float* pent_w = F + 6579456;
   float* ptv_w  = F + 6579584;
+  float* psum_w  = F + 6579712;
+  float* hidp_w  = F + 6841856;
+  float* pdel4_w = F + 7104000;
   unsigned short* Bsw_w = (unsigned short*)kapT_w;
   float* KmwT_w = kapT_w;
   float* kp_w   = fp_w;
-  float* psum_w = fp_w;
-  float* hidp_w = fp_w + 262144;
-  float* pdel4_w = gate_w;
 
   k_fused1 <<<Bn, 256, 0, stream>>>(text, W_t2k, b_t2k, mu_w, kapT_w, rr_w, ytr_w, pent_w, ptv_w);
   k_kemb1  <<<Bn*8, 128, 0, stream>>>(kapT_w, W_kemb, kp_w);
-  k_kemb2  <<<Bn, 256, 0, stream>>>(kp_w, b_kemb, kn_w);
-  k_wprep  <<<384, 256, 0, stream>>>(W_fp, Bsw_w);
-  k_encmean<<<Bn*8, 256, 0, stream>>>(enc, psum_w);
-  k_gmlp1  <<<1024, 256, 0, stream>>>(psum_w, text, vproj, W_g1, hidp_w);
-  k_gmlp2  <<<256, 256, 0, stream>>>(hidp_w, b_g1, W_g2, b_g2, gate_w);
-  k_fposm  <<<Bn*FTILES, 256, 0, stream>>>(yfut, Bsw_w, b_fp, fp_w, fi_w);
-  k_mse    <<<MSEB, 256, 0, stream>>>(y_res, yfut, gate_w, ytr_w, W_tir, b_tir, vproj, pmse_w);
-  k_cost   <<<Bn*4, 256, 0, stream>>>(kn_w, fp_w, fi_w, mu_w, KmwT_w);
+  k_p3     <<<1536, 256, 0, stream>>>(kp_w, b_kemb, kn_w, W_fp, Bsw_w, enc, psum_w);
+  k_p4     <<<1920, 256, 0, stream>>>(psum_w, text, vproj, W_g1, hidp_w,
+                                      yfut, Bsw_w, b_fp, fp_w, fi_w);
+  k_p5     <<<768, 256, 0, stream>>>(hidp_w, b_g1, W_g2, b_g2, gate_w,
+                                     kn_w, fp_w, fi_w, mu_w, KmwT_w);
   k_sink1w <<<Bn, 128, 0, stream>>>(rr_w, KmwT_w, pcot_w);
-  k_agg    <<<Bn*4, 256, 0, stream>>>(kn_w, fp_w, KmwT_w, perm, pdel4_w);
+  k_p7     <<<1536, 256, 0, stream>>>(y_res, yfut, gate_w, ytr_w, W_tir, b_tir, vproj,
+                                      pmse_w, kn_w, fp_w, KmwT_w, perm, pdel4_w);
   k_final  <<<1, 256, 0, stream>>>(pmse_w, pcot_w, pdel4_w, pent_w, ptv_w, (float*)d_out);
 }
```

New measurement: 326.2 us. -5.7%, faster.
